# Kernel tuning notes

Hardware: AMD Instinct MI355X
Metric: run time of the kernel (lower is better)

## Reference

```python
import jax, jax.numpy as jnp
import numpy as np

SIM = 100      # topk k
GCH = SIM + 1  # group size after concat
LCH = 80       # low-rank mid channels
D = 96         # embed dim


def setup_inputs() -> dict:
    key = jax.random.key(0)
    ks = jax.random.split(key, 14)
    b, N, W, p = 1, 4, 16, 128
    def lin(kw, kb, out_f, in_f):
        s = 1.0 / np.sqrt(in_f)
        w = jax.random.uniform(kw, (out_f, in_f), minval=-s, maxval=s, dtype=jnp.float32)
        bb = jax.random.uniform(kb, (out_f,), minval=-s, maxval=s, dtype=jnp.float32)
        return w, bb
    attn = jax.random.normal(ks[0], (b, N, W, 1, p, p), dtype=jnp.float32)
    v = jax.random.normal(ks[1], (b, N, W, 1, p, D), dtype=jnp.float32)
    mb = jax.random.normal(ks[2], (LCH, 1), dtype=jnp.float32)
    w_sub, b_sub = lin(ks[3], ks[4], LCH, GCH)
    w_up, b_up = lin(ks[5], ks[6], GCH, LCH)
    w_q, b_q = lin(ks[7], ks[8], D, D)
    w_k, b_k = lin(ks[9], ks[10], D, D)
    w_o, b_o = lin(ks[11], ks[12], D, D)
    return {"attn": attn, "v": v, "mb": mb, "w_sub": w_sub, "b_sub": b_sub,
            "w_up": w_up, "b_up": b_up, "w_q": w_q, "b_q": b_q,
            "w_k": w_k, "b_k": b_k, "w_o": w_o, "b_o": b_o}


def reference(attn, v, mb, w_sub, b_sub, w_up, b_up, w_q, b_q, w_k, b_k, w_o, b_o):
    b, N, W, _, p, _ = attn.shape
    c = v.shape[-1]
    # topk + scatter(binary mask) + boolean-compact gather == gather v rows at
    # ascending-sorted topk indices (boolean masking preserves index order).
    _, idx = jax.lax.top_k(attn, SIM)            # [b,N,W,1,p,SIM]
    idx = jnp.sort(idx[:, :, :, 0], axis=-1)     # [b,N,W,p,SIM]
    vq = v[:, :, :, 0]                            # [b,N,W,p,c]
    bI = jnp.arange(b)[:, None, None, None, None]
    nI = jnp.arange(N)[None, :, None, None, None]
    wI = jnp.arange(W)[None, None, :, None, None]
    gathered = vq[bI, nI, wI, idx]                # [b,N,W,p,SIM,c]
    group3d = jnp.concatenate([vq[:, :, :, :, None, :], gathered], axis=4)  # [b,N,W,p,GCH,c]
    # ChannelAttention (memory_blocks=1): pool over c, low-rank memory bank
    y = jnp.mean(group3d, axis=-1)                # [b,N,W,p,GCH]
    lr = y @ w_sub.T + b_sub                      # [b,N,W,p,LCH]
    f1 = (lr @ mb) * (LCH ** -0.5)                # [b,N,W,p,1]
    f_dic = jax.nn.softmax(f1[..., None, :], axis=-1)   # [b,N,W,p,1,1] == 1
    y1 = f_dic * mb[:, 0]                         # [b,N,W,p,1,LCH]
    scale = jax.nn.sigmoid(y1 @ w_up.T + b_up)    # [b,N,W,p,1,GCH]
    scale = scale.reshape(b, N, W, p, GCH, 1)     # matches torch .view(b,N,Nwin,p,n,-1)
    g = group3d * scale
    # StructuralSelfAttention (num_heads=1): query = group element 0, keys/values = rest
    x = g[:, :, :, :, :1, :]                      # [b,N,W,p,1,c]
    yk = g[:, :, :, :, 1:, :]                     # [b,N,W,p,SIM,c]
    q = x @ w_q.T + b_q
    k = yk @ w_k.T + b_k
    scores = jnp.einsum('bnwpqc,bnwpkc->bnwpqk', q, k) / jnp.sqrt(jnp.float32(c))
    wgt = jax.nn.softmax(scores, axis=-1)
    out = jnp.einsum('bnwpqk,bnwpkc->bnwpqc', wgt, yk)  # v = y (no v_proj in source)
    out = out.reshape(b, N, W, p, c)
    return out @ w_o.T + b_o
```

## Files before the change

### kernel.cpp

```cpp
#include <hip/hip_runtime.h>
#include <hip/hip_bf16.h>

#define NW 64
#define P 128
#define D 96
#define PD (P*D)
#define GCH 101
#define SIM 100
#define LCH 80
#define RSQRT96 0.10206207261596577f

#define WS_SCALE 0
#define WS_Q     128
#define WS_KT    (128 + 786432)
#define WS_VO    (128 + 2*786432)

typedef unsigned long long ull;

__device__ __forceinline__ ull make_key(float a, int idx) {
  unsigned u = __float_as_uint(a);
  unsigned msk = (u & 0x80000000u) ? 0xFFFFFFFFu : 0x80000000u;
  return (((ull)(u ^ msk)) << 32) | (unsigned)(127 - idx);
}

__global__ __launch_bounds__(128, 4) void proj_kernel(const float* __restrict__ v,
    const float* __restrict__ wq, const float* __restrict__ bq,
    const float* __restrict__ wk, const float* __restrict__ wo,
    const float* __restrict__ mb, const float* __restrict__ w_up,
    const float* __restrict__ b_up, float* __restrict__ ws) {
  int bid = blockIdx.x;
  int nw = bid / 6;
  int rem = bid - nw * 6;
  int pj = rem >> 1, rh = rem & 1;
  const float* W = (pj == 0) ? wq : (pj == 1) ? wk : wo;
  __shared__ float sWt[96 * 100];
  __shared__ float sV[64 * 97];
  int t = threadIdx.x;
  int ty = t >> 3;
  int tx = t & 7;

  for (int k = 0; k < 72; ++k) {
    int idx = t + 128 * k;
    int c = idx / 96, d = idx - c * 96;
    sWt[d * 100 + c] = W[idx];
  }
  const float* Vg = v + (size_t)nw * PD + rh * (64 * D);
#pragma unroll
  for (int i = 0; i < 12; ++i) {
    int idx = (t + 128 * i) * 4;
    float4 x = *(const float4*)(Vg + idx);
    int r = idx / 96, d = idx - r * 96;
    float* p = &sV[r * 97 + d];
    p[0] = x.x; p[1] = x.y; p[2] = x.z; p[3] = x.w;
  }
  float scale0 = 0.f;
  if (pj == 0) {
    float a = b_up[0];
    for (int j = 0; j < LCH; ++j) a += w_up[j] * mb[j];
    scale0 = 1.f / (1.f + __expf(-a));
  }
  __syncthreads();

  float acc[4][12];
#pragma unroll
  for (int a = 0; a < 4; ++a)
#pragma unroll
    for (int j = 0; j < 12; ++j) acc[a][j] = 0.f;

  for (int d = 0; d < 96; ++d) {
    float va0 = sV[(ty * 4 + 0) * 97 + d];
    float va1 = sV[(ty * 4 + 1) * 97 + d];
    float va2 = sV[(ty * 4 + 2) * 97 + d];
    float va3 = sV[(ty * 4 + 3) * 97 + d];
    const float4* wp = (const float4*)&sWt[d * 100 + tx * 12];
    float4 w0 = wp[0], w1 = wp[1], w2 = wp[2];
    float wb[12] = {w0.x,w0.y,w0.z,w0.w, w1.x,w1.y,w1.z,w1.w, w2.x,w2.y,w2.z,w2.w};
#pragma unroll
    for (int j = 0; j < 12; ++j) {
      acc[0][j] += va0 * wb[j];
      acc[1][j] += va1 * wb[j];
      acc[2][j] += va2 * wb[j];
      acc[3][j] += va3 * wb[j];
    }
  }

  if (pj == 1) {
    float* ktp = ws + WS_KT + nw * PD;
#pragma unroll
    for (int a = 0; a < 4; ++a) {
      int r = rh * 64 + ty * 4 + a;
#pragma unroll
      for (int j = 0; j < 12; ++j)
        ktp[(tx * 12 + j) * P + r] = acc[a][j];
    }
  } else {
    float* outp = ws + ((pj == 0) ? WS_Q : WS_VO) + nw * PD + (rh * 64) * D;
    float4 bq4[3];
    if (pj == 0) {
      const float4* bp = (const float4*)(bq + tx * 12);
      bq4[0] = bp[0]; bq4[1] = bp[1]; bq4[2] = bp[2];
    }
#pragma unroll
    for (int a = 0; a < 4; ++a) {
      float* orow = outp + (ty * 4 + a) * D + tx * 12;
#pragma unroll
      for (int q = 0; q < 3; ++q) {
        float4 o;
        o.x = acc[a][4*q+0]; o.y = acc[a][4*q+1];
        o.z = acc[a][4*q+2]; o.w = acc[a][4*q+3];
        if (pj == 0) {
          o.x = scale0 * o.x + bq4[q].x; o.y = scale0 * o.y + bq4[q].y;
          o.z = scale0 * o.z + bq4[q].z; o.w = scale0 * o.w + bq4[q].w;
        }
        *(float4*)(orow + 4 * q) = o;
      }
    }
  }

  if (bid == 0 && t < GCH) {
    float a = b_up[t];
    for (int j = 0; j < LCH; ++j) a += w_up[t * LCH + j] * mb[j];
    ws[WS_SCALE + t] = 1.f / (1.f + __expf(-a));
  }
}

__global__ __launch_bounds__(64, 2) void attn_kernel(const float* __restrict__ attn,
    const float* __restrict__ bo, const float* __restrict__ ws,
    float* __restrict__ out) {
  int lane = threadIdx.x;
  int nw = blockIdx.x >> 5;
  int p0 = (blockIdx.x & 31) << 2;
  const float* Kt  = ws + WS_KT + nw * PD;
  const float* VO  = ws + WS_VO + nw * PD;
  const float* Qb  = ws + WS_Q  + nw * PD + p0 * D;
  const float* Ab  = attn + (size_t)(nw * P + p0) * P;
  const float* scl = ws + WS_SCALE;

  ull k0[4], k1[4];
#pragma unroll
  for (int r = 0; r < 4; ++r) {
    k0[r] = make_key(Ab[r * P + lane], lane);
    k1[r] = make_key(Ab[r * P + 64 + lane], 64 + lane);
  }

  int c0_[4] = {0,0,0,0}, c1_[4] = {0,0,0,0};
  for (int jb = 0; jb < P; jb += 8) {
    float aj[4][8];
#pragma unroll
    for (int rr = 0; rr < 4; ++rr)
#pragma unroll
      for (int i = 0; i < 8; ++i) aj[rr][i] = Ab[rr * P + jb + i];
#pragma unroll
    for (int i = 0; i < 8; ++i) {
      int j = jb + i;
#pragma unroll
      for (int rr = 0; rr < 4; ++rr) {
        ull kj = make_key(aj[rr][i], j);
        c0_[rr] += (kj > k0[rr]) ? 1 : 0;
        c1_[rr] += (kj > k1[rr]) ? 1 : 0;
      }
    }
  }

  float s0[4] = {0,0,0,0}, s1[4] = {0,0,0,0};
  for (int cb = 0; cb < D; cb += 8) {
    float q[4][8];
#pragma unroll
    for (int rr = 0; rr < 4; ++rr)
#pragma unroll
      for (int i = 0; i < 8; ++i) q[rr][i] = Qb[rr * D + cb + i];
#pragma unroll
    for (int i = 0; i < 8; ++i) {
      int c = cb + i;
      float kv0 = Kt[c * P + lane];
      float kv1 = Kt[c * P + 64 + lane];
#pragma unroll
      for (int rr = 0; rr < 4; ++rr) {
        s0[rr] += q[rr][i] * kv0;
        s1[rr] += q[rr][i] * kv1;
      }
    }
  }

  float t0[4], t1[4];
  ull lm = (1ull << lane) - 1ull;
#pragma unroll
  for (int rr = 0; rr < 4; ++rr) {
    bool kp0 = c0_[rr] < SIM, kp1 = c1_[rr] < SIM;
    ull b0 = __ballot(kp0), b1 = __ballot(kp1);
    int pos0 = __popcll(b0 & lm);
    int pos1 = __popcll(b0) + __popcll(b1 & lm);
    float sv0 = kp0 ? scl[1 + pos0] : 0.f;
    float sv1 = kp1 ? scl[1 + pos1] : 0.f;
    float x0 = kp0 ? sv0 * s0[rr] * RSQRT96 : -1e30f;
    float x1 = kp1 ? sv1 * s1[rr] * RSQRT96 : -1e30f;
    float m = fmaxf(x0, x1);
#pragma unroll
    for (int off = 1; off < 64; off <<= 1) m = fmaxf(m, __shfl_xor(m, off));
    float e0 = kp0 ? __expf(x0 - m) : 0.f;
    float e1 = kp1 ? __expf(x1 - m) : 0.f;
    float s = e0 + e1;
#pragma unroll
    for (int off = 1; off < 64; off <<= 1) s += __shfl_xor(s, off);
    float inv = 1.f / s;
    t0[rr] = e0 * inv * sv0;
    t1[rr] = e1 * inv * sv1;
  }

  float o0[4] = {0,0,0,0}, o1[4] = {0,0,0,0};
  int lane2 = (lane < 32) ? (64 + lane) : 95;
#pragma unroll 4
  for (int j = 0; j < 64; ++j) {
    float vo0 = VO[j * D + lane];
    float vo1 = VO[j * D + lane2];
#pragma unroll
    for (int rr = 0; rr < 4; ++rr) {
      float tv = __int_as_float(__builtin_amdgcn_readlane(__float_as_int(t0[rr]), j));
      o0[rr] += tv * vo0;
      o1[rr] += tv * vo1;
    }
  }
#pragma unroll 4
  for (int j = 0; j < 64; ++j) {
    float vo0 = VO[(64 + j) * D + lane];
    float vo1 = VO[(64 + j) * D + lane2];
#pragma unroll
    for (int rr = 0; rr < 4; ++rr) {
      float tv = __int_as_float(__builtin_amdgcn_readlane(__float_as_int(t1[rr]), j));
      o0[rr] += tv * vo0;
      o1[rr] += tv * vo1;
    }
  }
  float bb0 = bo[lane];
  float bb1 = bo[lane2];
  float* op = out + (size_t)(nw * P + p0) * D;
#pragma unroll
  for (int rr = 0; rr < 4; ++rr) {
    op[rr * D + lane] = o0[rr] + bb0;
    if (lane < 32) op[rr * D + 64 + lane] = o1[rr] + bb1;
  }
}

extern "C" void kernel_launch(void* const* d_in, const int* in_sizes, int n_in,
                              void* d_out, int out_size, void* d_ws, size_t ws_size,
                              hipStream_t stream) {
  const float* attn = (const float*)d_in[0];
  const float* v    = (const float*)d_in[1];
  const float* mb   = (const float*)d_in[2];
  const float* w_up = (const float*)d_in[5];
  const float* b_up = (const float*)d_in[6];
  const float* w_q  = (const float*)d_in[7];
  const float* b_q  = (const float*)d_in[8];
  const float* w_k  = (const float*)d_in[9];
  const float* w_o  = (const float*)d_in[11];
  const float* b_o  = (const float*)d_in[12];
  float* out = (float*)d_out;
  float* ws = (float*)d_ws;

  hipLaunchKernelGGL(proj_kernel, dim3(NW * 6), dim3(128), 0, stream,
                     v, w_q, b_q, w_k, w_o, mb, w_up, b_up, ws);
  hipLaunchKernelGGL(attn_kernel, dim3(NW * 32), dim3(64), 0, stream,
                     attn, b_o, ws, out);
}
```

Before: 67.77 us.

## Halve per-block work and remap blocks so each XCD handles whole windows

Both kernels are split finer: projection blocks now cover 32 rows instead of 64, and attention blocks cover 2 query rows instead of 4, which doubles the grid sizes. Block indices are remapped so blocks sharing a window land on the same XCD (bid & 7), aiming to improve L2 reuse of per-window K/V/Q data. The attention kernel also switches to float2 interleaved even/odd column layout with a single 128-step PV loop. The cost is more redundant weight loads and less per-block register reuse.

```diff
diff --git a/kernel.cpp b/kernel.cpp
--- a/kernel.cpp
+++ b/kernel.cpp
@@ -23,18 +23,21 @@
   return (((ull)(u ^ msk)) << 32) | (unsigned)(127 - idx);
 }
 
-__global__ __launch_bounds__(128, 4) void proj_kernel(const float* __restrict__ v,
+__global__ __launch_bounds__(128, 2) void proj_kernel(const float* __restrict__ v,
     const float* __restrict__ wq, const float* __restrict__ bq,
     const float* __restrict__ wk, const float* __restrict__ wo,
     const float* __restrict__ mb, const float* __restrict__ w_up,
     const float* __restrict__ b_up, float* __restrict__ ws) {
   int bid = blockIdx.x;
-  int nw = bid / 6;
-  int rem = bid - nw * 6;
-  int pj = rem >> 1, rh = rem & 1;
+  int xcd = bid & 7;
+  int m = bid >> 3;
+  int g = m / 12;
+  int rem = m - g * 12;
+  int nw = (g << 3) | xcd;
+  int pj = rem >> 2, rh = rem & 3;
   const float* W = (pj == 0) ? wq : (pj == 1) ? wk : wo;
   __shared__ float sWt[96 * 100];
-  __shared__ float sV[64 * 97];
+  __shared__ float sV[32 * 97];
   int t = threadIdx.x;
   int ty = t >> 3;
   int tx = t & 7;
@@ -44,9 +47,9 @@
     int c = idx / 96, d = idx - c * 96;
     sWt[d * 100 + c] = W[idx];
   }
-  const float* Vg = v + (size_t)nw * PD + rh * (64 * D);
-#pragma unroll
-  for (int i = 0; i < 12; ++i) {
+  const float* Vg = v + (size_t)nw * PD + rh * (32 * D);
+#pragma unroll
+  for (int i = 0; i < 6; ++i) {
     int idx = (t + 128 * i) * 4;
     float4 x = *(const float4*)(Vg + idx);
     int r = idx / 96, d = idx - r * 96;
@@ -61,17 +64,15 @@
   }
   __syncthreads();
 
-  float acc[4][12];
-#pragma unroll
-  for (int a = 0; a < 4; ++a)
+  float acc[2][12];
+#pragma unroll
+  for (int a = 0; a < 2; ++a)
 #pragma unroll
     for (int j = 0; j < 12; ++j) acc[a][j] = 0.f;
 
   for (int d = 0; d < 96; ++d) {
-    float va0 = sV[(ty * 4 + 0) * 97 + d];
-    float va1 = sV[(ty * 4 + 1) * 97 + d];
-    float va2 = sV[(ty * 4 + 2) * 97 + d];
-    float va3 = sV[(ty * 4 + 3) * 97 + d];
+    float va0 = sV[(ty * 2 + 0) * 97 + d];
+    float va1 = sV[(ty * 2 + 1) * 97 + d];
     const float4* wp = (const float4*)&sWt[d * 100 + tx * 12];
     float4 w0 = wp[0], w1 = wp[1], w2 = wp[2];
     float wb[12] = {w0.x,w0.y,w0.z,w0.w, w1.x,w1.y,w1.z,w1.w, w2.x,w2.y,w2.z,w2.w};
@@ -79,30 +80,28 @@
     for (int j = 0; j < 12; ++j) {
       acc[0][j] += va0 * wb[j];
       acc[1][j] += va1 * wb[j];
-      acc[2][j] += va2 * wb[j];
-      acc[3][j] += va3 * wb[j];
     }
   }
 
   if (pj == 1) {
     float* ktp = ws + WS_KT + nw * PD;
 #pragma unroll
-    for (int a = 0; a < 4; ++a) {
-      int r = rh * 64 + ty * 4 + a;
+    for (int a = 0; a < 2; ++a) {
+      int r = rh * 32 + ty * 2 + a;
 #pragma unroll
       for (int j = 0; j < 12; ++j)
         ktp[(tx * 12 + j) * P + r] = acc[a][j];
     }
   } else {
-    float* outp = ws + ((pj == 0) ? WS_Q : WS_VO) + nw * PD + (rh * 64) * D;
+    float* outp = ws + ((pj == 0) ? WS_Q : WS_VO) + nw * PD + (rh * 32) * D;
     float4 bq4[3];
     if (pj == 0) {
       const float4* bp = (const float4*)(bq + tx * 12);
       bq4[0] = bp[0]; bq4[1] = bp[1]; bq4[2] = bp[2];
     }
 #pragma unroll
-    for (int a = 0; a < 4; ++a) {
-      float* orow = outp + (ty * 4 + a) * D + tx * 12;
+    for (int a = 0; a < 2; ++a) {
+      float* orow = outp + (ty * 2 + a) * D + tx * 12;
 #pragma unroll
       for (int q = 0; q < 3; ++q) {
         float4 o;
@@ -124,120 +123,111 @@
   }
 }
 
-__global__ __launch_bounds__(64, 2) void attn_kernel(const float* __restrict__ attn,
+__global__ __launch_bounds__(64, 4) void attn_kernel(const float* __restrict__ attn,
     const float* __restrict__ bo, const float* __restrict__ ws,
     float* __restrict__ out) {
+  int bid = blockIdx.x;
   int lane = threadIdx.x;
-  int nw = blockIdx.x >> 5;
-  int p0 = (blockIdx.x & 31) << 2;
+  int xcd = bid & 7;
+  int nw = ((bid >> 9) << 3) | xcd;
+  int rt = (bid >> 3) & 63;
+  int p0 = rt * 2;
   const float* Kt  = ws + WS_KT + nw * PD;
   const float* VO  = ws + WS_VO + nw * PD;
   const float* Qb  = ws + WS_Q  + nw * PD + p0 * D;
   const float* Ab  = attn + (size_t)(nw * P + p0) * P;
   const float* scl = ws + WS_SCALE;
 
-  ull k0[4], k1[4];
-#pragma unroll
-  for (int r = 0; r < 4; ++r) {
-    k0[r] = make_key(Ab[r * P + lane], lane);
-    k1[r] = make_key(Ab[r * P + 64 + lane], 64 + lane);
-  }
-
-  int c0_[4] = {0,0,0,0}, c1_[4] = {0,0,0,0};
+  ull ke[2], ko[2];
+#pragma unroll
+  for (int r = 0; r < 2; ++r) {
+    float2 a2 = ((const float2*)(Ab + r * P))[lane];
+    ke[r] = make_key(a2.x, 2 * lane);
+    ko[r] = make_key(a2.y, 2 * lane + 1);
+  }
+
+  int ce[2] = {0, 0}, co_[2] = {0, 0};
   for (int jb = 0; jb < P; jb += 8) {
-    float aj[4][8];
-#pragma unroll
-    for (int rr = 0; rr < 4; ++rr)
-#pragma unroll
-      for (int i = 0; i < 8; ++i) aj[rr][i] = Ab[rr * P + jb + i];
+    float aj[2][8];
+#pragma unroll
+    for (int r = 0; r < 2; ++r)
+#pragma unroll
+      for (int i = 0; i < 8; ++i) aj[r][i] = Ab[r * P + jb + i];
 #pragma unroll
     for (int i = 0; i < 8; ++i) {
       int j = jb + i;
 #pragma unroll
-      for (int rr = 0; rr < 4; ++rr) {
-        ull kj = make_key(aj[rr][i], j);
-        c0_[rr] += (kj > k0[rr]) ? 1 : 0;
-        c1_[rr] += (kj > k1[rr]) ? 1 : 0;
+      for (int r = 0; r < 2; ++r) {
+        ull kj = make_key(aj[r][i], j);
+        ce[r]  += (kj > ke[r]) ? 1 : 0;
+        co_[r] += (kj > ko[r]) ? 1 : 0;
       }
     }
   }
 
-  float s0[4] = {0,0,0,0}, s1[4] = {0,0,0,0};
+  float se[2] = {0, 0}, so[2] = {0, 0};
   for (int cb = 0; cb < D; cb += 8) {
-    float q[4][8];
-#pragma unroll
-    for (int rr = 0; rr < 4; ++rr)
-#pragma unroll
-      for (int i = 0; i < 8; ++i) q[rr][i] = Qb[rr * D + cb + i];
+    float q[2][8];
+#pragma unroll
+    for (int r = 0; r < 2; ++r)
+#pragma unroll
+      for (int i = 0; i < 8; ++i) q[r][i] = Qb[r * D + cb + i];
 #pragma unroll
     for (int i = 0; i < 8; ++i) {
-      int c = cb + i;
-      float kv0 = Kt[c * P + lane];
-      float kv1 = Kt[c * P + 64 + lane];
-#pragma unroll
-      for (int rr = 0; rr < 4; ++rr) {
-        s0[rr] += q[rr][i] * kv0;
-        s1[rr] += q[rr][i] * kv1;
+      float2 kv = ((const float2*)(Kt + (cb + i) * P))[lane];
+#pragma unroll
+      for (int r = 0; r < 2; ++r) {
+        se[r] += q[r][i] * kv.x;
+        so[r] += q[r][i] * kv.y;
       }
     }
   }
 
-  float t0[4], t1[4];
+  float te[2], to[2];
   ull lm = (1ull << lane) - 1ull;
 #pragma unroll
-  for (int rr = 0; rr < 4; ++rr) {
-    bool kp0 = c0_[rr] < SIM, kp1 = c1_[rr] < SIM;
-    ull b0 = __ballot(kp0), b1 = __ballot(kp1);
-    int pos0 = __popcll(b0 & lm);
-    int pos1 = __popcll(b0) + __popcll(b1 & lm);
-    float sv0 = kp0 ? scl[1 + pos0] : 0.f;
-    float sv1 = kp1 ? scl[1 + pos1] : 0.f;
-    float x0 = kp0 ? sv0 * s0[rr] * RSQRT96 : -1e30f;
-    float x1 = kp1 ? sv1 * s1[rr] * RSQRT96 : -1e30f;
-    float m = fmaxf(x0, x1);
-#pragma unroll
-    for (int off = 1; off < 64; off <<= 1) m = fmaxf(m, __shfl_xor(m, off));
-    float e0 = kp0 ? __expf(x0 - m) : 0.f;
-    float e1 = kp1 ? __expf(x1 - m) : 0.f;
-    float s = e0 + e1;
+  for (int r = 0; r < 2; ++r) {
+    bool kpe = ce[r] < SIM, kpo = co_[r] < SIM;
+    ull be = __ballot(kpe), bo_ = __ballot(kpo);
+    int pe = __popcll(be & lm) + __popcll(bo_ & lm);
+    int po = pe + (kpe ? 1 : 0);
+    float sve = kpe ? scl[1 + pe] : 0.f;
+    float svo = kpo ? scl[1 + po] : 0.f;
+    float xe = kpe ? sve * se[r] * RSQRT96 : -1e30f;
+    float xo = kpo ? svo * so[r] * RSQRT96 : -1e30f;
+    float mx = fmaxf(xe, xo);
+#pragma unroll
+    for (int off = 1; off < 64; off <<= 1) mx = fmaxf(mx, __shfl_xor(mx, off));
+    float ee = kpe ? __expf(xe - mx) : 0.f;
+    float eo = kpo ? __expf(xo - mx) : 0.f;
+    float s = ee + eo;
 #pragma unroll
     for (int off = 1; off < 64; off <<= 1) s += __shfl_xor(s, off);
     float inv = 1.f / s;
-    t0[rr] = e0 * inv * sv0;
-    t1[rr] = e1 * inv * sv1;
-  }
-
-  float o0[4] = {0,0,0,0}, o1[4] = {0,0,0,0};
-  int lane2 = (lane < 32) ? (64 + lane) : 95;
-#pragma unroll 4
-  for (int j = 0; j < 64; ++j) {
-    float vo0 = VO[j * D + lane];
-    float vo1 = VO[j * D + lane2];
-#pragma unroll
-    for (int rr = 0; rr < 4; ++rr) {
-      float tv = __int_as_float(__builtin_amdgcn_readlane(__float_as_int(t0[rr]), j));
-      o0[rr] += tv * vo0;
-      o1[rr] += tv * vo1;
-    }
-  }
-#pragma unroll 4
-  for (int j = 0; j < 64; ++j) {
-    float vo0 = VO[(64 + j) * D + lane];
-    float vo1 = VO[(64 + j) * D + lane2];
-#pragma unroll
-    for (int rr = 0; rr < 4; ++rr) {
-      float tv = __int_as_float(__builtin_amdgcn_readlane(__float_as_int(t1[rr]), j));
-      o0[rr] += tv * vo0;
-      o1[rr] += tv * vo1;
-    }
-  }
-  float bb0 = bo[lane];
-  float bb1 = bo[lane2];
-  float* op = out + (size_t)(nw * P + p0) * D;
-#pragma unroll
-  for (int rr = 0; rr < 4; ++rr) {
-    op[rr * D + lane] = o0[rr] + bb0;
-    if (lane < 32) op[rr * D + 64 + lane] = o1[rr] + bb1;
+    te[r] = ee * inv * sve;
+    to[r] = eo * inv * svo;
+  }
+
+  int lc = (lane < 48) ? lane : 47;
+  float2 o0 = {0.f, 0.f}, o1 = {0.f, 0.f};
+#pragma unroll 8
+  for (int j = 0; j < P; ++j) {
+    float2 vo = ((const float2*)(VO + j * D))[lc];
+    int h = j >> 1;
+    float tv0 = __int_as_float(__builtin_amdgcn_readlane(
+        __float_as_int((j & 1) ? to[0] : te[0]), h));
+    float tv1 = __int_as_float(__builtin_amdgcn_readlane(
+        __float_as_int((j & 1) ? to[1] : te[1]), h));
+    o0.x += tv0 * vo.x; o0.y += tv0 * vo.y;
+    o1.x += tv1 * vo.x; o1.y += tv1 * vo.y;
+  }
+  if (lane < 48) {
+    float2 bb = ((const float2*)bo)[lane];
+    float* op = out + (size_t)(nw * P + p0) * D;
+    float2 r0; r0.x = o0.x + bb.x; r0.y = o0.y + bb.y;
+    float2 r1; r1.x = o1.x + bb.x; r1.y = o1.y + bb.y;
+    ((float2*)(op + 0 * D))[lane] = r0;
+    ((float2*)(op + 1 * D))[lane] = r1;
   }
 }
 
@@ -257,8 +247,8 @@
   float* out = (float*)d_out;
   float* ws = (float*)d_ws;
 
-  hipLaunchKernelGGL(proj_kernel, dim3(NW * 6), dim3(128), 0, stream,
+  hipLaunchKernelGGL(proj_kernel, dim3(768), dim3(128), 0, stream,
                      v, w_q, b_q, w_k, w_o, mb, w_up, b_up, ws);
-  hipLaunchKernelGGL(attn_kernel, dim3(NW * 32), dim3(64), 0, stream,
+  hipLaunchKernelGGL(attn_kernel, dim3(4096), dim3(64), 0, stream,
                      attn, b_o, ws, out);
 }
```

New measurement: 96.43 us. 42.3% more time.
